# Performance work log

Measured on AMD Instinct MI355X. Metric: run time of the kernel, lower is better.

## Reference

```python
import jax, jax.numpy as jnp
import numpy as np

NUM_USERS, NUM_ITEMS, NUM_GROUPS = 100000, 50000, 20000
D = 64
B, M = 16384, 50


def setup_inputs() -> dict:
    key = jax.random.key(0)
    ks = jax.random.split(key, 16)
    inp = {
        "group_inputs": jax.random.randint(ks[0], (B,), 0, NUM_GROUPS),
        "item_inputs": jax.random.randint(ks[1], (B,), 0, NUM_ITEMS),
        "member_ids": jax.random.randint(ks[2], (B, M), 0, NUM_USERS),
        "member_lengths": jax.random.randint(ks[3], (B,), 0, M),
        # embedding tables (xavier-ish scale)
        "user_table": jax.random.normal(ks[4], (NUM_USERS, D), jnp.float32) * 0.05,
        "item_table": jax.random.normal(ks[5], (NUM_ITEMS, D), jnp.float32) * 0.05,
        "group_table": jax.random.normal(ks[6], (NUM_GROUPS, D), jnp.float32) * 0.05,
        # attention MLP: 2D -> 16 -> 1
        "att_w1": jax.random.normal(ks[7], (2 * D, 16), jnp.float32) * 0.1,
        "att_b1": jnp.zeros((16,), jnp.float32),
        "att_w2": jax.random.normal(ks[8], (16, 1), jnp.float32) * 0.1,
        "att_b2": jnp.zeros((1,), jnp.float32),
        # predict MLP: 3D -> 8 -> 1
        "pred_w1": jax.random.normal(ks[9], (3 * D, 8), jnp.float32) * 0.1,
        "pred_b1": jnp.zeros((8,), jnp.float32),
        "pred_w2": jax.random.normal(ks[10], (8, 1), jnp.float32) * 0.1,
        "pred_b2": jnp.zeros((1,), jnp.float32),
    }
    return inp


def reference(group_inputs, item_inputs, member_ids, member_lengths,
              user_table, item_table, group_table,
              att_w1, att_b1, att_w2, att_b2,
              pred_w1, pred_b1, pred_w2, pred_b2):
    # mask: at least one valid member per group
    mask = jnp.arange(M)[None, :] <= member_lengths[:, None]          # [B, M] bool
    mem_e = user_table[member_ids]                                    # [B, M, D]
    item_e = item_table[item_inputs]                                  # [B, D]

    # attention over members: concat(member, item) -> 16 -> 1
    gi = jnp.concatenate(
        [mem_e, jnp.broadcast_to(item_e[:, None, :], mem_e.shape)], axis=-1)  # [B, M, 2D]
    h = jax.nn.relu(jnp.einsum('bmk,kh->bmh', gi, att_w1) + att_b1)   # [B, M, 16]
    scores = (jnp.einsum('bmh,ho->bmo', h, att_w2) + att_b2)[..., 0]  # [B, M]
    scores = jnp.where(mask, scores, -jnp.inf)
    at_wt = jax.nn.softmax(scores, axis=-1)                           # [B, M]

    g_att = jnp.einsum('bm,bmd->bd', at_wt, mem_e)                    # [B, D]
    g = g_att + group_table[group_inputs]                             # [B, D]

    elem = g * item_e
    new_e = jnp.concatenate([elem, g, item_e], axis=-1)               # [B, 3D]
    ph = jax.nn.relu(new_e @ pred_w1 + pred_b1)                       # [B, 8]
    y = jax.nn.sigmoid(ph @ pred_w2 + pred_b2)                        # [B, 1]
    return y
```

## Files before the change

kernel.cpp:

```cpp
#include <hip/hip_runtime.h>
#include <math.h>

constexpr int MM = 50;
constexpr int DD = 64;
constexpr int HH = 16;
constexpr int PH = 8;
constexpr int WAVES_PER_BLOCK = 4;
constexpr int SLOTS = 56;

__device__ __forceinline__ unsigned bf16rne(float f) {
    const unsigned u = __float_as_uint(f);
    return (u + 0x7FFFu + ((u >> 16) & 1u)) >> 16;
}

__global__ __launch_bounds__(256) void precompute_kernel(
    const float* __restrict__ user_table,
    const float* __restrict__ item_table,
    const int*   __restrict__ item_inputs,
    const float* __restrict__ att_w1,
    const float* __restrict__ att_b1,
    unsigned short* __restrict__ Ubf,
    float* __restrict__ Ib,
    unsigned short* __restrict__ Ub,
    int nU, int B, int userBlocks)
{
    const bool isU = (int)blockIdx.x < userBlocks;
    const float4* rp;
    const float*  w1;
    float acc[HH];
    int row = 0;

    if (isU) {
        row = (int)blockIdx.x * 256 + (int)threadIdx.x;
        if (row >= nU) return;
        rp  = (const float4*)(user_table + (size_t)row * DD);
        w1  = att_w1;
        #pragma unroll
        for (int j = 0; j < HH; ++j) acc[j] = 0.0f;
    } else {
        row = ((int)blockIdx.x - userBlocks) * 256 + (int)threadIdx.x;
        if (row >= B) return;
        const int item = item_inputs[row];
        rp  = (const float4*)(item_table + (size_t)item * DD);
        w1  = att_w1 + (size_t)DD * HH;
        #pragma unroll
        for (int j = 0; j < HH; ++j) acc[j] = att_b1[j];
    }

    unsigned brow[DD / 2];

    #pragma unroll 4
    for (int d4 = 0; d4 < DD / 4; ++d4) {
        const float4 x = rp[d4];
        const float* w = w1 + (size_t)(d4 * 4) * HH;
        #pragma unroll
        for (int j = 0; j < HH; ++j) {
            acc[j] = fmaf(x.x, w[0 * HH + j], acc[j]);
            acc[j] = fmaf(x.y, w[1 * HH + j], acc[j]);
            acc[j] = fmaf(x.z, w[2 * HH + j], acc[j]);
            acc[j] = fmaf(x.w, w[3 * HH + j], acc[j]);
        }
        brow[2 * d4]     = bf16rne(x.x) | (bf16rne(x.y) << 16);
        brow[2 * d4 + 1] = bf16rne(x.z) | (bf16rne(x.w) << 16);
    }

    if (isU) {
        unsigned uw[8];
        #pragma unroll
        for (int w = 0; w < 8; ++w)
            uw[w] = bf16rne(acc[2 * w]) | (bf16rne(acc[2 * w + 1]) << 16);
        uint4* u4 = (uint4*)(Ubf + (size_t)row * HH);
        u4[0] = make_uint4(uw[0], uw[1], uw[2], uw[3]);
        u4[1] = make_uint4(uw[4], uw[5], uw[6], uw[7]);

        uint4* b4 = (uint4*)(Ub + (size_t)row * DD);
        #pragma unroll
        for (int i = 0; i < DD / 8; ++i)
            b4[i] = make_uint4(brow[4 * i], brow[4 * i + 1],
                               brow[4 * i + 2], brow[4 * i + 3]);
    } else {
        float4* o4 = (float4*)(Ib + (size_t)row * HH);
        o4[0] = make_float4(acc[0],  acc[1],  acc[2],  acc[3]);
        o4[1] = make_float4(acc[4],  acc[5],  acc[6],  acc[7]);
        o4[2] = make_float4(acc[8],  acc[9],  acc[10], acc[11]);
        o4[3] = make_float4(acc[12], acc[13], acc[14], acc[15]);
    }
}

__global__ __launch_bounds__(256) void agree_main(
    const int* __restrict__ group_inputs,
    const int* __restrict__ item_inputs,
    const int* __restrict__ member_ids,
    const int* __restrict__ member_lengths,
    const float* __restrict__ item_table,
    const float* __restrict__ group_table,
    const float* __restrict__ att_w2,
    const float* __restrict__ att_b2,
    const float* __restrict__ pred_w1,
    const float* __restrict__ pred_b1,
    const float* __restrict__ pred_w2,
    const float* __restrict__ pred_b2,
    const unsigned short* __restrict__ Ubf,
    const float* __restrict__ Ib,
    const unsigned short* __restrict__ Ub,
    float* __restrict__ out,
    int B)
{
    __shared__ float2 pairs[WAVES_PER_BLOCK][SLOTS];

    const int lane = threadIdx.x & 63;
    const int wv   = threadIdx.x >> 6;
    const int b    = blockIdx.x * WAVES_PER_BLOCK + wv;
    if (b >= B) return;

    const int my_m  = (lane < MM) ? lane : (MM - 1);
    const int my_id = member_ids[b * MM + my_m];
    const int len   = member_lengths[b];
    const int item_idx = item_inputs[b];
    const int gid      = group_inputs[b];

    const float item_d = item_table[(unsigned)(item_idx * DD + lane)];
    const float grp_d  = group_table[(unsigned)(gid * DD + lane)];

    const uint4* up = (const uint4*)(Ubf + ((size_t)(unsigned)my_id * HH));
    const uint4 ua = up[0], ubw = up[1];
    const float* ib = Ib + (size_t)b * HH;

    float score = att_b2[0];
    {
        const unsigned uw[8] = { ua.x, ua.y, ua.z, ua.w,
                                 ubw.x, ubw.y, ubw.z, ubw.w };
        #pragma unroll
        for (int w = 0; w < 8; ++w) {
            const float f0 = __uint_as_float(uw[w] << 16);
            const float f1 = __uint_as_float(uw[w] & 0xFFFF0000u);
            score = fmaf(fmaxf(f0 + ib[2 * w],     0.0f), att_w2[2 * w],     score);
            score = fmaf(fmaxf(f1 + ib[2 * w + 1], 0.0f), att_w2[2 * w + 1], score);
        }
    }

    const bool valid = (lane < MM) && (lane <= len);
    score = valid ? score : -INFINITY;

    float mx = score;
    #pragma unroll
    for (int off = 32; off > 0; off >>= 1) mx = fmaxf(mx, __shfl_xor(mx, off, 64));
    const float e = valid ? __expf(score - mx) : 0.0f;
    float sum = e;
    #pragma unroll
    for (int off = 32; off > 0; off >>= 1) sum += __shfl_xor(sum, off, 64);
    const float wnorm = e / sum;

    if (lane < SLOTS) pairs[wv][lane] = make_float2(wnorm, __int_as_float(my_id));
    __builtin_amdgcn_s_waitcnt(0);

    const int mcnt   = (len < MM - 1 ? len : MM - 1) + 1;
    const int chunks = (mcnt + 7) >> 3;

    float g = 0.0f;
    for (int c = 0; c < chunks; ++c) {
        float2 q[8];
        #pragma unroll
        for (int k = 0; k < 8; ++k) q[k] = pairs[wv][c * 8 + k];
        unsigned short xb[8];
        #pragma unroll
        for (int k = 0; k < 8; ++k) {
            const unsigned idx = (unsigned)(__float_as_int(q[k].y) * DD + lane);
            xb[k] = Ub[idx];
        }
        #pragma unroll
        for (int k = 0; k < 8; ++k)
            g = fmaf(q[k].x, __uint_as_float((unsigned)xb[k] << 16), g);
    }
    g += grp_d;

    const float elem = g * item_d;
    float p[PH];
    {
        const float* pa = pred_w1 + (size_t)lane * PH;
        const float* pb = pred_w1 + (size_t)(DD + lane) * PH;
        const float* pc = pred_w1 + (size_t)(2 * DD + lane) * PH;
        #pragma unroll
        for (int j = 0; j < PH; ++j)
            p[j] = fmaf(elem, pa[j], fmaf(g, pb[j], item_d * pc[j]));
    }
    #pragma unroll
    for (int off = 32; off > 0; off >>= 1) {
        #pragma unroll
        for (int j = 0; j < PH; ++j) p[j] += __shfl_xor(p[j], off, 64);
    }

    if (lane == 0) {
        float acc = pred_b2[0];
        #pragma unroll
        for (int j = 0; j < PH; ++j)
            acc = fmaf(fmaxf(p[j] + pred_b1[j], 0.0f), pred_w2[j], acc);
        out[b] = 1.0f / (1.0f + __expf(-acc));
    }
}

__global__ __launch_bounds__(256) void agree_fallback(
    const int* __restrict__ group_inputs,
    const int* __restrict__ item_inputs,
    const int* __restrict__ member_ids,
    const int* __restrict__ member_lengths,
    const float* __restrict__ user_table,
    const float* __restrict__ item_table,
    const float* __restrict__ group_table,
    const float* __restrict__ att_w1,
    const float* __restrict__ att_b1,
    const float* __restrict__ att_w2,
    const float* __restrict__ att_b2,
    const float* __restrict__ pred_w1,
    const float* __restrict__ pred_b1,
    const float* __restrict__ pred_w2,
    const float* __restrict__ pred_b2,
    float* __restrict__ out,
    int B)
{
    __shared__ float lds_wt[4][MM];
    __shared__ int   lds_id[4][MM];

    const int lane = threadIdx.x & 63;
    const int wave = threadIdx.x >> 6;
    const int b = blockIdx.x * 4 + wave;
    if (b >= B) return;

    const int my_m = (lane < MM) ? lane : (MM - 1);
    const int my_id = member_ids[b * MM + my_m];
    if (lane < MM) lds_id[wave][lane] = my_id;

    const int item_idx = item_inputs[b];
    const float item_d = item_table[(size_t)item_idx * DD + lane];

    float h[HH];
    {
        const float* w1row = att_w1 + (size_t)(DD + lane) * HH;
        #pragma unroll
        for (int j = 0; j < HH; ++j) h[j] = item_d * w1row[j];
        #pragma unroll
        for (int off = 32; off > 0; off >>= 1) {
            #pragma unroll
            for (int j = 0; j < HH; ++j) h[j] += __shfl_xor(h[j], off, 64);
        }
        #pragma unroll
        for (int j = 0; j < HH; ++j) h[j] += att_b1[j];
    }

    const float* myrow = user_table + (size_t)my_id * DD;
    #pragma unroll 4
    for (int d4 = 0; d4 < DD / 4; ++d4) {
        const float4 x = ((const float4*)myrow)[d4];
        const float* w1d = att_w1 + (size_t)(d4 * 4) * HH;
        #pragma unroll
        for (int j = 0; j < HH; ++j) {
            h[j] = fmaf(x.x, w1d[0 * HH + j], h[j]);
            h[j] = fmaf(x.y, w1d[1 * HH + j], h[j]);
            h[j] = fmaf(x.z, w1d[2 * HH + j], h[j]);
            h[j] = fmaf(x.w, w1d[3 * HH + j], h[j]);
        }
    }

    float score = att_b2[0];
    #pragma unroll
    for (int j = 0; j < HH; ++j) score = fmaf(fmaxf(h[j], 0.0f), att_w2[j], score);

    const int len = member_lengths[b];
    const bool valid = (lane < MM) && (lane <= len);
    score = valid ? score : -INFINITY;

    float mx = score;
    #pragma unroll
    for (int off = 32; off > 0; off >>= 1) mx = fmaxf(mx, __shfl_xor(mx, off, 64));
    float e = valid ? __expf(score - mx) : 0.0f;
    float sum = e;
    #pragma unroll
    for (int off = 32; off > 0; off >>= 1) sum += __shfl_xor(sum, off, 64);
    if (lane < MM) lds_wt[wave][lane] = e / sum;
    __builtin_amdgcn_s_waitcnt(0);

    const int mcnt = (len < MM - 1 ? len : MM - 1) + 1;
    float g = 0.0f;
    #pragma unroll 2
    for (int m = 0; m < mcnt; ++m) {
        g = fmaf(lds_wt[wave][m],
                 user_table[(size_t)lds_id[wave][m] * DD + lane], g);
    }
    const int gid = group_inputs[b];
    g += group_table[(size_t)gid * DD + lane];

    const float elem = g * item_d;
    float p[PH];
    {
        const float* pa = pred_w1 + (size_t)lane * PH;
        const float* pb = pred_w1 + (size_t)(DD + lane) * PH;
        const float* pc = pred_w1 + (size_t)(2 * DD + lane) * PH;
        #pragma unroll
        for (int j = 0; j < PH; ++j)
            p[j] = fmaf(elem, pa[j], fmaf(g, pb[j], item_d * pc[j]));
    }
    #pragma unroll
    for (int off = 32; off > 0; off >>= 1) {
        #pragma unroll
        for (int j = 0; j < PH; ++j) p[j] += __shfl_xor(p[j], off, 64);
    }

    if (lane == 0) {
        float acc = pred_b2[0];
        #pragma unroll
        for (int j = 0; j < PH; ++j)
            acc = fmaf(fmaxf(p[j] + pred_b1[j], 0.0f), pred_w2[j], acc);
        out[b] = 1.0f / (1.0f + __expf(-acc));
    }
}

extern "C" void kernel_launch(void* const* d_in, const int* in_sizes, int n_in,
                              void* d_out, int out_size, void* d_ws, size_t ws_size,
                              hipStream_t stream) {
    const int*   group_inputs   = (const int*)d_in[0];
    const int*   item_inputs    = (const int*)d_in[1];
    const int*   member_ids     = (const int*)d_in[2];
    const int*   member_lengths = (const int*)d_in[3];
    const float* user_table     = (const float*)d_in[4];
    const float* item_table     = (const float*)d_in[5];
    const float* group_table    = (const float*)d_in[6];
    const float* att_w1         = (const float*)d_in[7];
    const float* att_b1         = (const float*)d_in[8];
    const float* att_w2         = (const float*)d_in[9];
    const float* att_b2         = (const float*)d_in[10];
    const float* pred_w1        = (const float*)d_in[11];
    const float* pred_b1        = (const float*)d_in[12];
    const float* pred_w2        = (const float*)d_in[13];
    const float* pred_b2        = (const float*)d_in[14];
    float* out = (float*)d_out;

    const int B  = in_sizes[0];
    const int nU = in_sizes[4] / DD;
    const size_t need = (size_t)nU * HH * sizeof(unsigned short)
                      + (size_t)B  * HH * sizeof(float)
                      + (size_t)nU * DD * sizeof(unsigned short);
    const int blocks = (B + WAVES_PER_BLOCK - 1) / WAVES_PER_BLOCK;

    if (ws_size >= need) {
        unsigned short* Ubf = (unsigned short*)d_ws;
        float* Ib = (float*)(Ubf + (size_t)nU * HH);
        unsigned short* Ub = (unsigned short*)(Ib + (size_t)B * HH);
        const int userBlocks = (nU + 255) / 256;
        const int itemBlocks = (B + 255) / 256;
        precompute_kernel<<<userBlocks + itemBlocks, 256, 0, stream>>>(
            user_table, item_table, item_inputs, att_w1, att_b1,
            Ubf, Ib, Ub, nU, B, userBlocks);
        agree_main<<<blocks, 256, 0, stream>>>(
            group_inputs, item_inputs, member_ids, member_lengths,
            item_table, group_table,
            att_w2, att_b2, pred_w1, pred_b1, pred_w2, pred_b2,
            Ubf, Ib, Ub, out, B);
    } else {
        agree_fallback<<<blocks, 256, 0, stream>>>(
            group_inputs, item_inputs, member_ids, member_lengths,
            user_table, item_table, group_table,
            att_w1, att_b1, att_w2, att_b2,
            pred_w1, pred_b1, pred_w2, pred_b2,
            out, B);
    }
}
```

Baseline: 143.4 us.

## Issue member row gathers before softmax via templated chunk count and shuffles

The main kernel is restructured so each wave issues all bf16 member-row gathers up front, before computing attention scores and softmax. Member ids and softmax weights are broadcast with wave shuffles instead of going through an LDS staging array. A switch on the chunk count picks a template instantiation, which makes the gather loop fully unrolled. This is meant to overlap gather latency with the score computation and remove the LDS round trip, at the cost of more registers for the xb buffer (up to 56 values) and a larger code footprint.

```diff
diff --git a/kernel.cpp b/kernel.cpp
--- a/kernel.cpp
+++ b/kernel.cpp
@@ -6,11 +6,13 @@
 constexpr int HH = 16;
 constexpr int PH = 8;
 constexpr int WAVES_PER_BLOCK = 4;
-constexpr int SLOTS = 56;
 
 __device__ __forceinline__ unsigned bf16rne(float f) {
     const unsigned u = __float_as_uint(f);
     return (u + 0x7FFFu + ((u >> 16) & 1u)) >> 16;
+}
+__device__ __forceinline__ float bf16tof(unsigned short v) {
+    return __uint_as_float((unsigned)v << 16);
 }
 
 __global__ __launch_bounds__(256) void precompute_kernel(
@@ -84,6 +86,86 @@
         o4[1] = make_float4(acc[4],  acc[5],  acc[6],  acc[7]);
         o4[2] = make_float4(acc[8],  acc[9],  acc[10], acc[11]);
         o4[3] = make_float4(acc[12], acc[13], acc[14], acc[15]);
+    }
+}
+
+template<int NC>
+__device__ __forceinline__ void agree_wave(
+    const unsigned short* __restrict__ Ubf,
+    const float* __restrict__ Ib,
+    const unsigned short* __restrict__ Ub,
+    const float* __restrict__ att_w2, const float* __restrict__ att_b2,
+    const float* __restrict__ pred_w1, const float* __restrict__ pred_b1,
+    const float* __restrict__ pred_w2, const float* __restrict__ pred_b2,
+    float* __restrict__ out,
+    int b, int lane, int my_id, int len, float item_d, float grp_d)
+{
+    const uint4* up = (const uint4*)(Ubf + ((size_t)(unsigned)my_id * HH));
+    const uint4 ua = up[0], ubw = up[1];
+
+    unsigned short xb[NC * 8];
+    #pragma unroll
+    for (int k = 0; k < NC * 8; ++k) {
+        const int idk = __shfl(my_id, k, 64);
+        xb[k] = Ub[(unsigned)(idk * DD + lane)];
+    }
+
+    const float* ib = Ib + (size_t)b * HH;
+    float score = att_b2[0];
+    {
+        const unsigned uw[8] = { ua.x, ua.y, ua.z, ua.w,
+                                 ubw.x, ubw.y, ubw.z, ubw.w };
+        #pragma unroll
+        for (int w = 0; w < 8; ++w) {
+            const float f0 = __uint_as_float(uw[w] << 16);
+            const float f1 = __uint_as_float(uw[w] & 0xFFFF0000u);
+            score = fmaf(fmaxf(f0 + ib[2 * w],     0.0f), att_w2[2 * w],     score);
+            score = fmaf(fmaxf(f1 + ib[2 * w + 1], 0.0f), att_w2[2 * w + 1], score);
+        }
+    }
+
+    const bool valid = (lane < MM) && (lane <= len);
+    score = valid ? score : -INFINITY;
+
+    float mx = score;
+    #pragma unroll
+    for (int off = 32; off > 0; off >>= 1) mx = fmaxf(mx, __shfl_xor(mx, off, 64));
+    const float e = valid ? __expf(score - mx) : 0.0f;
+    float sum = e;
+    #pragma unroll
+    for (int off = 32; off > 0; off >>= 1) sum += __shfl_xor(sum, off, 64);
+    const float wnorm = e / sum;
+
+    float g = 0.0f;
+    #pragma unroll
+    for (int k = 0; k < NC * 8; ++k) {
+        const float wk = __shfl(wnorm, k, 64);
+        g = fmaf(wk, bf16tof(xb[k]), g);
+    }
+    g += grp_d;
+
+    const float elem = g * item_d;
+    float p[PH];
+    {
+        const float* pa = pred_w1 + (size_t)lane * PH;
+        const float* pb = pred_w1 + (size_t)(DD + lane) * PH;
+        const float* pc = pred_w1 + (size_t)(2 * DD + lane) * PH;
+        #pragma unroll
+        for (int j = 0; j < PH; ++j)
+            p[j] = fmaf(elem, pa[j], fmaf(g, pb[j], item_d * pc[j]));
+    }
+    #pragma unroll
+    for (int off = 32; off > 0; off >>= 1) {
+        #pragma unroll
+        for (int j = 0; j < PH; ++j) p[j] += __shfl_xor(p[j], off, 64);
+    }
+
+    if (lane == 0) {
+        float acc = pred_b2[0];
+        #pragma unroll
+        for (int j = 0; j < PH; ++j)
+            acc = fmaf(fmaxf(p[j] + pred_b1[j], 0.0f), pred_w2[j], acc);
+        out[b] = 1.0f / (1.0f + __expf(-acc));
     }
 }
 
@@ -106,8 +188,6 @@
     float* __restrict__ out,
     int B)
 {
-    __shared__ float2 pairs[WAVES_PER_BLOCK][SLOTS];
-
     const int lane = threadIdx.x & 63;
     const int wv   = threadIdx.x >> 6;
     const int b    = blockIdx.x * WAVES_PER_BLOCK + wv;
@@ -122,80 +202,24 @@
     const float item_d = item_table[(unsigned)(item_idx * DD + lane)];
     const float grp_d  = group_table[(unsigned)(gid * DD + lane)];
 
-    const uint4* up = (const uint4*)(Ubf + ((size_t)(unsigned)my_id * HH));
-    const uint4 ua = up[0], ubw = up[1];
-    const float* ib = Ib + (size_t)b * HH;
-
-    float score = att_b2[0];
-    {
-        const unsigned uw[8] = { ua.x, ua.y, ua.z, ua.w,
-                                 ubw.x, ubw.y, ubw.z, ubw.w };
-        #pragma unroll
-        for (int w = 0; w < 8; ++w) {
-            const float f0 = __uint_as_float(uw[w] << 16);
-            const float f1 = __uint_as_float(uw[w] & 0xFFFF0000u);
-            score = fmaf(fmaxf(f0 + ib[2 * w],     0.0f), att_w2[2 * w],     score);
-            score = fmaf(fmaxf(f1 + ib[2 * w + 1], 0.0f), att_w2[2 * w + 1], score);
-        }
-    }
-
-    const bool valid = (lane < MM) && (lane <= len);
-    score = valid ? score : -INFINITY;
-
-    float mx = score;
-    #pragma unroll
-    for (int off = 32; off > 0; off >>= 1) mx = fmaxf(mx, __shfl_xor(mx, off, 64));
-    const float e = valid ? __expf(score - mx) : 0.0f;
-    float sum = e;
-    #pragma unroll
-    for (int off = 32; off > 0; off >>= 1) sum += __shfl_xor(sum, off, 64);
-    const float wnorm = e / sum;
-
-    if (lane < SLOTS) pairs[wv][lane] = make_float2(wnorm, __int_as_float(my_id));
-    __builtin_amdgcn_s_waitcnt(0);
-
     const int mcnt   = (len < MM - 1 ? len : MM - 1) + 1;
     const int chunks = (mcnt + 7) >> 3;
 
-    float g = 0.0f;
-    for (int c = 0; c < chunks; ++c) {
-        float2 q[8];
-        #pragma unroll
-        for (int k = 0; k < 8; ++k) q[k] = pairs[wv][c * 8 + k];
-        unsigned short xb[8];
-        #pragma unroll
-        for (int k = 0; k < 8; ++k) {
-            const unsigned idx = (unsigned)(__float_as_int(q[k].y) * DD + lane);
-            xb[k] = Ub[idx];
-        }
-        #pragma unroll
-        for (int k = 0; k < 8; ++k)
-            g = fmaf(q[k].x, __uint_as_float((unsigned)xb[k] << 16), g);
-    }
-    g += grp_d;
-
-    const float elem = g * item_d;
-    float p[PH];
-    {
-        const float* pa = pred_w1 + (size_t)lane * PH;
-        const float* pb = pred_w1 + (size_t)(DD + lane) * PH;
-        const float* pc = pred_w1 + (size_t)(2 * DD + lane) * PH;
-        #pragma unroll
-        for (int j = 0; j < PH; ++j)
-            p[j] = fmaf(elem, pa[j], fmaf(g, pb[j], item_d * pc[j]));
-    }
-    #pragma unroll
-    for (int off = 32; off > 0; off >>= 1) {
-        #pragma unroll
-        for (int j = 0; j < PH; ++j) p[j] += __shfl_xor(p[j], off, 64);
-    }
-
-    if (lane == 0) {
-        float acc = pred_b2[0];
-        #pragma unroll
-        for (int j = 0; j < PH; ++j)
-            acc = fmaf(fmaxf(p[j] + pred_b1[j], 0.0f), pred_w2[j], acc);
-        out[b] = 1.0f / (1.0f + __expf(-acc));
+    switch (chunks) {
+    case 1: agree_wave<1>(Ubf, Ib, Ub, att_w2, att_b2, pred_w1, pred_b1,
+                          pred_w2, pred_b2, out, b, lane, my_id, len, item_d, grp_d); break;
+    case 2: agree_wave<2>(Ubf, Ib, Ub, att_w2, att_b2, pred_w1, pred_b1,
+                          pred_w2, pred_b2, out, b, lane, my_id, len, item_d, grp_d); break;
+    case 3: agree_wave<3>(Ubf, Ib, Ub, att_w2, att_b2, pred_w1, pred_b1,
+                          pred_w2, pred_b2, out, b, lane, my_id, len, item_d, grp_d); break;
+    case 4: agree_wave<4>(Ubf, Ib, Ub, att_w2, att_b2, pred_w1, pred_b1,
+                          pred_w2, pred_b2, out, b, lane, my_id, len, item_d, grp_d); break;
+    case 5: agree_wave<5>(Ubf, Ib, Ub, att_w2, att_b2, pred_w1, pred_b1,
+                          pred_w2, pred_b2, out, b, lane, my_id, len, item_d, grp_d); break;
+    case 6: agree_wave<6>(Ubf, Ib, Ub, att_w2, att_b2, pred_w1, pred_b1,
+                          pred_w2, pred_b2, out, b, lane, my_id, len, item_d, grp_d); break;
+    default: agree_wave<7>(Ubf, Ib, Ub, att_w2, att_b2, pred_w1, pred_b1,
+                           pred_w2, pred_b2, out, b, lane, my_id, len, item_d, grp_d); break;
     }
 }
 
```

Measured after the change: 146.0 us. No clear change (+1.9%).
